# Optimization experiments

Measured on AMD Instinct MI355X. Metric: run time of the kernel, lower is better.

The kernel has to match this reference:

```python
import jax, jax.numpy as jnp
import numpy as np
import math

B, C_IN, C_OUT, W, H = 16, 64, 64, 256, 128
KW = 7  # conv kernel (1, 7), valid padding -> H' = H - 6


def _conv(x, w, b):
    # NCHW input, OIHW weight, valid padding, stride 1 (matches nn.Conv2d)
    y = jax.lax.conv_general_dilated(x, w, (1, 1), 'VALID',
                                     dimension_numbers=('NCHW', 'OIHW', 'NCHW'))
    return y + b[None, :, None, None]


def setup_inputs() -> dict:
    key = jax.random.key(0)
    ks = jax.random.split(key, 7)
    scale = 1.0 / math.sqrt(C_IN * KW)
    x = jax.random.normal(ks[0], (B, C_IN, W, H), jnp.float32)
    wK = jax.random.normal(ks[1], (C_OUT, C_IN, 1, KW), jnp.float32) * scale
    bK = jax.random.normal(ks[2], (C_OUT,), jnp.float32) * scale
    wQ = jax.random.normal(ks[3], (C_OUT, C_IN, 1, KW), jnp.float32) * scale
    bQ = jax.random.normal(ks[4], (C_OUT,), jnp.float32) * scale
    wV = jax.random.normal(ks[5], (C_OUT, C_IN, 1, KW), jnp.float32) * scale
    bV = jax.random.normal(ks[6], (C_OUT,), jnp.float32) * scale
    return {'x': x, 'wK': wK, 'bK': bK, 'wQ': wQ, 'bQ': bQ, 'wV': wV, 'bV': bV}


def reference(x, wK, bK, wQ, bQ, wV, bV):
    b, c, w, h = x.shape
    # raw row-major flatten of NCHW conv output into (B, W, C*H') -- faithful
    # to torch's .reshape(nbatches, w, -1) on a contiguous tensor
    k = _conv(x, wK, bK).reshape(b, w, -1)   # [B, W, C_OUT*(H-6)]
    q = _conv(x, wQ, bQ).reshape(b, w, -1)   # [B, W, C_OUT*(H-6)]
    v = x.reshape(b, w, -1)                  # [B, W, C_IN*H]
    d_k = q.shape[-1]
    scores = jnp.einsum('bqd,bkd->bqk', q, k) / math.sqrt(d_k)  # [B, W, W]
    i = jnp.arange(w)[:, None]
    j = jnp.arange(w)[None, :]
    blocked = ((i < 128) & (j < 128)) | ((i >= 128) & (j >= 128))
    scores = jnp.where(blocked, -jnp.inf, scores)
    p = jax.nn.softmax(scores, axis=-1)
    x1 = jnp.einsum('bqk,bkd->bqd', p, v).reshape(b, c, w, h)
    y = _conv(x1 + x, wV, bV)                # [B, C_OUT, W, H-6]
    return jnp.where(y >= 0, y, 0.2 * y)     # LeakyReLU(0.2)
```

## Files before the change

### kernel.cpp

```cpp
#include <hip/hip_runtime.h>
#include <hip/hip_bf16.h>

using uint32 = unsigned int;
using u16 = unsigned short;
using short8 = __attribute__((ext_vector_type(8))) short;
using f32x4  = __attribute__((ext_vector_type(4))) float;

__device__ __forceinline__ float bf2f(u16 u) {
  union { uint32 i; float f; } c; c.i = ((uint32)u) << 16; return c.f;
}
__device__ __forceinline__ u16 f2bf(float f) {
  union { float f; uint32 i; } c; c.f = f;
  uint32 u = c.i;
  u += 0x7fffu + ((u >> 16) & 1u);
  return (u16)(u >> 16);
}
__device__ __forceinline__ uint32 pack2(float a, float b) {
  return (uint32)f2bf(a) | ((uint32)f2bf(b) << 16);
}

__device__ __forceinline__ void gload_lds16(const void* g, void* l) {
  __builtin_amdgcn_global_load_lds(
      (const __attribute__((address_space(1))) unsigned int*)g,
      (__attribute__((address_space(3))) unsigned int*)l, 16, 0, 0);
}


__global__ __launch_bounds__(256) void prep_weights(
    const float* __restrict__ wK, const float* __restrict__ wQ,
    const float* __restrict__ wV,
    u16* __restrict__ pK, u16* __restrict__ pQ, u16* __restrict__ pV)
{
  int idx = blockIdx.x * 256 + threadIdx.x;
  if (idx >= 86016) return;
  int set = idx / 28672;
  int r = idx - set * 28672;
  int kw = r >> 12;
  int rem = r & 4095;
  int co = rem >> 6, ci = rem & 63;
  const float* src = set == 0 ? wK : (set == 1 ? wQ : wV);
  u16* dst = set == 0 ? pK : (set == 1 ? pQ : pV);
  dst[r] = f2bf(src[co * 448 + ci * 7 + kw]);
}

__global__ __launch_bounds__(256) void prep_x(
    const float* __restrict__ x, u16* __restrict__ xbuf)
{
  __shared__ u16 xt[128 * 64];
  const int bid = blockIdx.x;
  const int b = bid >> 8, w = bid & 255;
  const int t = threadIdx.x;
  const float* xb = x + (size_t)b * 2097152 + (size_t)w * 128;
  #pragma unroll
  for (int it = 0; it < 8; ++it) {
    int idx = t + it * 256;
    int h = idx & 127, gq = idx >> 7;
    int ci0 = gq * 4;
    float v0 = xb[(size_t)(ci0 + 0) * 32768 + h];
    float v1 = xb[(size_t)(ci0 + 1) * 32768 + h];
    float v2 = xb[(size_t)(ci0 + 2) * 32768 + h];
    float v3 = xb[(size_t)(ci0 + 3) * 32768 + h];
    uint2 pk; pk.x = pack2(v0, v1); pk.y = pack2(v2, v3);
    int col = ci0 ^ ((h & 7) << 3);
    *reinterpret_cast<uint2*>(&xt[h * 64 + col]) = pk;
  }
  __syncthreads();
  const uint4* s = reinterpret_cast<const uint4*>(xt);
  uint4* d = reinterpret_cast<uint4*>(xbuf + (size_t)bid * 8192);
  #pragma unroll
  for (int it = 0; it < 4; ++it) d[t + it * 256] = s[t + it * 256];
}

__global__ __launch_bounds__(256) void prep_z(
    const u16* __restrict__ zraw, u16* __restrict__ ztbuf)
{
  __shared__ u16 xt[128 * 64];
  const int bid = blockIdx.x;
  const int b = bid >> 8, w = bid & 255;
  const int t = threadIdx.x;
  const u16* zb = zraw + (size_t)b * 2097152 + (size_t)w * 128;
  #pragma unroll
  for (int it = 0; it < 8; ++it) {
    int idx = t + it * 256;
    int h = idx & 127, gq = idx >> 7;
    int ci0 = gq * 4;
    u16 v0 = zb[(size_t)(ci0 + 0) * 32768 + h];
    u16 v1 = zb[(size_t)(ci0 + 1) * 32768 + h];
    u16 v2 = zb[(size_t)(ci0 + 2) * 32768 + h];
    u16 v3 = zb[(size_t)(ci0 + 3) * 32768 + h];
    uint2 pk;
    pk.x = (uint32)v0 | ((uint32)v1 << 16);
    pk.y = (uint32)v2 | ((uint32)v3 << 16);
    int col = ci0 ^ ((h & 7) << 3);
    *reinterpret_cast<uint2*>(&xt[h * 64 + col]) = pk;
  }
  __syncthreads();
  const uint4* s = reinterpret_cast<const uint4*>(xt);
  uint4* d = reinterpret_cast<uint4*>(ztbuf + (size_t)bid * 8192);
  #pragma unroll
  for (int it = 0; it < 4; ++it) d[t + it * 256] = s[t + it * 256];
}

__global__ __launch_bounds__(256, 4) void conv_kq_mfma(
    const u16* __restrict__ xbuf,
    const u16* __restrict__ wpK, const u16* __restrict__ wpQ,
    const float* __restrict__ bK, const float* __restrict__ bQ,
    u16* __restrict__ qbuf, u16* __restrict__ kbuf)
{
  __shared__ u16 xt[136 * 64];
  const int bid = blockIdx.x;
  const int b = bid >> 8, w = bid & 255;
  const int t = threadIdx.x;
  const int lane = t & 63, wv = t >> 6;
  const int ln = lane & 15, g = lane >> 4;

  {
    const u16* src = xbuf + (size_t)bid * 8192;
    #pragma unroll
    for (int c = 0; c < 4; ++c) {
      int chunk = wv * 4 + c;
      gload_lds16(src + chunk * 512 + lane * 8, &xt[chunk * 512]);
    }
    if (t < 128) {
      *reinterpret_cast<uint2*>(&xt[128 * 64 + t * 4]) = make_uint2(0u, 0u);
    }
  }
  asm volatile("s_waitcnt vmcnt(0)" ::: "memory");
  __syncthreads();

  f32x4 accK[8], accQ[8];
  #pragma unroll
  for (int j = 0; j < 8; ++j) { accK[j] = (f32x4)0.f; accQ[j] = (f32x4)0.f; }

  for (int kw = 0; kw < 7; ++kw) {
    #pragma unroll
    for (int ks = 0; ks < 2; ++ks) {
      const int kb = ks * 32 + g * 8;
      const size_t woff = (size_t)(kw * 64 + wv * 16 + ln) * 64 + kb;
      short8 aK = *reinterpret_cast<const short8*>(wpK + woff);
      short8 aQ = *reinterpret_cast<const short8*>(wpQ + woff);
      #pragma unroll
      for (int j = 0; j < 8; ++j) {
        int row = j * 16 + ln + kw;
        int col = kb ^ ((row & 7) << 3);
        short8 bf = *reinterpret_cast<const short8*>(&xt[row * 64 + col]);
        accK[j] = __builtin_amdgcn_mfma_f32_16x16x32_bf16(aK, bf, accK[j], 0, 0, 0);
        accQ[j] = __builtin_amdgcn_mfma_f32_16x16x32_bf16(aQ, bf, accQ[j], 0, 0, 0);
      }
    }
  }

  #pragma unroll
  for (int r = 0; r < 4; ++r) {
    int co = wv * 16 + g * 4 + r;
    float bk = bK[co], bq = bQ[co];
    size_t base = ((size_t)(b * 64 + co) * 256 + w) * 122;
    #pragma unroll
    for (int j = 0; j < 8; ++j) {
      int n = j * 16 + ln;
      if (n < 122) {
        kbuf[base + n] = f2bf(accK[j][r] + bk);
        qbuf[base + n] = f2bf(accQ[j][r] + bq);
      }
    }
  }
}

__global__ __launch_bounds__(256) void scores_mfma(
    const u16* __restrict__ qbuf, const u16* __restrict__ kbuf,
    u16* __restrict__ pbuf)
{
  __shared__ float lmax[4][16];
  __shared__ float lsum[4][16];
  const int bid = blockIdx.x;
  const int b = bid & 15, rt = bid >> 4;
  const int t = threadIdx.x;
  const int lane = t & 63, wq = t >> 6;
  const int g = lane >> 4, ln = lane & 15;
  const int i0 = rt * 16;
  const int jbase = (rt < 8) ? 128 : 0;

  const u16* qp  = qbuf + (size_t)(b * 256 + i0 + ln) * 7808 + g * 8;
  const u16* kp0 = kbuf + (size_t)(b * 256 + jbase + wq * 32 + ln) * 7808 + g * 8;
  const u16* kp1 = kp0 + (size_t)16 * 7808;

  f32x4 acc0 = (f32x4)0.f, acc1 = (f32x4)0.f;
  #pragma unroll 4
  for (int c = 0; c < 244; ++c) {
    short8 af = *reinterpret_cast<const short8*>(qp + c * 32);
    short8 b0 = *reinterpret_cast<const short8*>(kp0 + c * 32);
    short8 b1 = *reinterpret_cast<const short8*>(kp1 + c * 32);
    acc0 = __builtin_amdgcn_mfma_f32_16x16x32_bf16(af, b0, acc0, 0, 0, 0);
    acc1 = __builtin_amdgcn_mfma_f32_16x16x32_bf16(af, b1, acc1, 0, 0, 0);
  }

  const float scale = 0.011316967f;
  float s0[4], s1[4];
  #pragma unroll
  for (int r = 0; r < 4; ++r) { s0[r] = acc0[r] * scale; s1[r] = acc1[r] * scale; }

  float pm[4], ps[4];
  #pragma unroll
  for (int r = 0; r < 4; ++r) {
    float m = fmaxf(s0[r], s1[r]);
    #pragma unroll
    for (int off = 8; off >= 1; off >>= 1) m = fmaxf(m, __shfl_xor(m, off));
    float e = __expf(s0[r] - m) + __expf(s1[r] - m);
    #pragma unroll
    for (int off = 8; off >= 1; off >>= 1) e += __shfl_xor(e, off);
    pm[r] = m; ps[r] = e;
  }
  if (ln == 0) {
    #pragma unroll
    for (int r = 0; r < 4; ++r) {
      lmax[wq][g * 4 + r] = pm[r];
      lsum[wq][g * 4 + r] = ps[r];
    }
  }
  __syncthreads();

  #pragma unroll
  for (int r = 0; r < 4; ++r) {
    int row = g * 4 + r;
    float m0 = lmax[0][row], m1 = lmax[1][row], m2 = lmax[2][row], m3 = lmax[3][row];
    float mm = fmaxf(fmaxf(m0, m1), fmaxf(m2, m3));
    float ss = lsum[0][row] * __expf(m0 - mm) + lsum[1][row] * __expf(m1 - mm)
             + lsum[2][row] * __expf(m2 - mm) + lsum[3][row] * __expf(m3 - mm);
    float inv = 1.0f / ss;
    float p0 = __expf(s0[r] - mm) * inv;
    float p1 = __expf(s1[r] - mm) * inv;
    u16* prow = pbuf + (size_t)(b * 256 + i0 + row) * 128 + wq * 32 + ln;
    prow[0]  = f2bf(p0);
    prow[16] = f2bf(p1);
  }
}

__global__ __launch_bounds__(256) void pv_mfma(
    const u16* __restrict__ pbuf, const float* __restrict__ x,
    u16* __restrict__ zraw)
{
  __shared__ u16 pl[128 * 136];
  __shared__ u16 vt[256 * 40];
  const int bid = blockIdx.x;
  const int b  = bid >> 6;
  const int hb = (bid >> 5) & 1;
  const int ec = bid & 31;
  const int t = threadIdx.x;
  const int lane = t & 63, wv = t >> 6;
  const int ln = lane & 15, g = lane >> 4;

  const int i0 = hb ? 0 : 128;
  const int jbase = hb ? 128 : 0;
  const int e0 = ec * 256;
  const float* xb = x + (size_t)b * 2097152;

  {
    const u16* pb = pbuf + (size_t)(b * 256 + i0) * 128;
    #pragma unroll
    for (int it = 0; it < 8; ++it) {
      int idx = t + it * 256;
      int row = idx >> 4, c = idx & 15;
      uint4 v = *reinterpret_cast<const uint4*>(pb + row * 128 + c * 8);
      *reinterpret_cast<uint4*>(&pl[row * 136 + c * 8]) = v;
    }
  }

  f32x4 acc[2][16];
  #pragma unroll
  for (int mt = 0; mt < 2; ++mt)
    #pragma unroll
    for (int nt = 0; nt < 16; ++nt) acc[mt][nt] = (f32x4)0.f;

  uint32* vtw = reinterpret_cast<uint32*>(vt);
  for (int ks = 0; ks < 4; ++ks) {
    __syncthreads();
    #pragma unroll
    for (int it = 0; it < 16; ++it) {
      int idx = t + it * 256;
      int e = idx & 255, jp = idx >> 8;
      const float* vr = xb + (size_t)(jbase + ks * 32 + jp * 2) * 8192 + e0 + e;
      float f0 = vr[0];
      float f1 = vr[8192];
      vtw[e * 20 + jp] = pack2(f0, f1);
    }
    __syncthreads();
    short8 af[2];
    #pragma unroll
    for (int mt = 0; mt < 2; ++mt) {
      int row = wv * 32 + mt * 16 + ln;
      af[mt] = *reinterpret_cast<const short8*>(&pl[row * 136 + ks * 32 + g * 8]);
    }
    #pragma unroll
    for (int nt = 0; nt < 16; ++nt) {
      int e = nt * 16 + ln;
      short8 bf = *reinterpret_cast<const short8*>(&vt[e * 40 + g * 8]);
      acc[0][nt] = __builtin_amdgcn_mfma_f32_16x16x32_bf16(af[0], bf, acc[0][nt], 0, 0, 0);
      acc[1][nt] = __builtin_amdgcn_mfma_f32_16x16x32_bf16(af[1], bf, acc[1][nt], 0, 0, 0);
    }
  }

  #pragma unroll
  for (int mt = 0; mt < 2; ++mt) {
    #pragma unroll
    for (int r = 0; r < 4; ++r) {
      int i = i0 + wv * 32 + mt * 16 + g * 4 + r;
      const float* xr = xb + (size_t)i * 8192 + e0 + ln;
      u16* zr = zraw + (size_t)(b * 256 + i) * 8192 + e0 + ln;
      #pragma unroll
      for (int nt = 0; nt < 16; ++nt) {
        float z = xr[nt * 16] + acc[mt][nt][r];
        zr[nt * 16] = f2bf(z);
      }
    }
  }
}

__global__ __launch_bounds__(256, 4) void conv_out_mfma(
    const u16* __restrict__ ztbuf, const u16* __restrict__ wpV,
    const float* __restrict__ bV, float* __restrict__ out)
{
  __shared__ u16 xt[136 * 64];
  const int bid = blockIdx.x;
  const int b = bid >> 8, w = bid & 255;
  const int t = threadIdx.x;
  const int lane = t & 63, wv = t >> 6;
  const int ln = lane & 15, g = lane >> 4;

  {
    const u16* src = ztbuf + (size_t)bid * 8192;
    #pragma unroll
    for (int c = 0; c < 4; ++c) {
      int chunk = wv * 4 + c;
      gload_lds16(src + chunk * 512 + lane * 8, &xt[chunk * 512]);
    }
    if (t < 128) {
      *reinterpret_cast<uint2*>(&xt[128 * 64 + t * 4]) = make_uint2(0u, 0u);
    }
  }
  asm volatile("s_waitcnt vmcnt(0)" ::: "memory");
  __syncthreads();

  f32x4 acc[8];
  #pragma unroll
  for (int j = 0; j < 8; ++j) acc[j] = (f32x4)0.f;

  for (int kw = 0; kw < 7; ++kw) {
    #pragma unroll
    for (int ks = 0; ks < 2; ++ks) {
      const int kb = ks * 32 + g * 8;
      const size_t woff = (size_t)(kw * 64 + wv * 16 + ln) * 64 + kb;
      short8 aV = *reinterpret_cast<const short8*>(wpV + woff);
      #pragma unroll
      for (int j = 0; j < 8; ++j) {
        int row = j * 16 + ln + kw;
        int col = kb ^ ((row & 7) << 3);
        short8 bf = *reinterpret_cast<const short8*>(&xt[row * 64 + col]);
        acc[j] = __builtin_amdgcn_mfma_f32_16x16x32_bf16(aV, bf, acc[j], 0, 0, 0);
      }
    }
  }

  #pragma unroll
  for (int r = 0; r < 4; ++r) {
    int co = wv * 16 + g * 4 + r;
    float bv = bV[co];
    size_t base = ((size_t)(b * 64 + co) * 256 + w) * 122;
    #pragma unroll
    for (int j = 0; j < 8; ++j) {
      int n = j * 16 + ln;
      if (n < 122) {
        float y = acc[j][r] + bv;
        out[base + n] = (y >= 0.f) ? y : 0.2f * y;
      }
    }
  }
}

extern "C" void kernel_launch(void* const* d_in, const int* in_sizes, int n_in,
                              void* d_out, int out_size, void* d_ws, size_t ws_size,
                              hipStream_t stream) {
  const float* x  = (const float*)d_in[0];
  const float* wK = (const float*)d_in[1];
  const float* bK = (const float*)d_in[2];
  const float* wQ = (const float*)d_in[3];
  const float* bQ = (const float*)d_in[4];
  const float* wV = (const float*)d_in[5];
  const float* bV = (const float*)d_in[6];
  float* out = (float*)d_out;

  char* ws = (char*)d_ws;
  u16* qbuf  = (u16*)ws;
  u16* pbuf  = (u16*)(ws + 63963136);
  u16* wpK   = (u16*)(ws + 65011712);
  u16* wpQ   = (u16*)(ws + 65069056);
  u16* kbuf  = (u16*)(ws + 65126400);
  u16* xbuf  = (u16*)(ws + 129089536);
  u16* zraw  = xbuf;
  u16* wpV   = (u16*)(ws + 196198400);
  u16* ztbuf = (u16*)ws;

  prep_weights<<<dim3(336), dim3(256), 0, stream>>>(wK, wQ, wV, wpK, wpQ, wpV);
  prep_x<<<dim3(16 * 256), dim3(256), 0, stream>>>(x, xbuf);
  conv_kq_mfma<<<dim3(16 * 256), dim3(256), 0, stream>>>(xbuf, wpK, wpQ, bK, bQ, qbuf, kbuf);
  scores_mfma<<<dim3(256), dim3(256), 0, stream>>>(qbuf, kbuf, pbuf);
  pv_mfma<<<dim3(1024), dim3(256), 0, stream>>>(pbuf, x, zraw);
  prep_z<<<dim3(16 * 256), dim3(256), 0, stream>>>(zraw, ztbuf);
  conv_out_mfma<<<dim3(16 * 256), dim3(256), 0, stream>>>(ztbuf, wpV, bV, out);
}
```

Measured before the change: 395.1 us.

## Fuse z transpose into PV epilogue and stage conv outputs through LDS

Drops the separate prep_z kernel. The PV kernel now writes its result, already transposed and swizzled, straight into the layout the output convolution consumes, staging each tile through shared memory. The K/Q conv and output conv epilogues also stage results in LDS so that global stores become contiguous wide writes instead of scattered 2-byte and 4-byte stores. This removes a full read and write pass over the z tensor and improves store coalescing, at the cost of extra barriers and LDS traffic in the epilogues. The workspace layout is also reshuffled.

```diff
diff --git a/kernel.cpp b/kernel.cpp
--- a/kernel.cpp
+++ b/kernel.cpp
@@ -67,36 +67,6 @@
   __syncthreads();
   const uint4* s = reinterpret_cast<const uint4*>(xt);
   uint4* d = reinterpret_cast<uint4*>(xbuf + (size_t)bid * 8192);
-  #pragma unroll
-  for (int it = 0; it < 4; ++it) d[t + it * 256] = s[t + it * 256];
-}
-
-__global__ __launch_bounds__(256) void prep_z(
-    const u16* __restrict__ zraw, u16* __restrict__ ztbuf)
-{
-  __shared__ u16 xt[128 * 64];
-  const int bid = blockIdx.x;
-  const int b = bid >> 8, w = bid & 255;
-  const int t = threadIdx.x;
-  const u16* zb = zraw + (size_t)b * 2097152 + (size_t)w * 128;
-  #pragma unroll
-  for (int it = 0; it < 8; ++it) {
-    int idx = t + it * 256;
-    int h = idx & 127, gq = idx >> 7;
-    int ci0 = gq * 4;
-    u16 v0 = zb[(size_t)(ci0 + 0) * 32768 + h];
-    u16 v1 = zb[(size_t)(ci0 + 1) * 32768 + h];
-    u16 v2 = zb[(size_t)(ci0 + 2) * 32768 + h];
-    u16 v3 = zb[(size_t)(ci0 + 3) * 32768 + h];
-    uint2 pk;
-    pk.x = (uint32)v0 | ((uint32)v1 << 16);
-    pk.y = (uint32)v2 | ((uint32)v3 << 16);
-    int col = ci0 ^ ((h & 7) << 3);
-    *reinterpret_cast<uint2*>(&xt[h * 64 + col]) = pk;
-  }
-  __syncthreads();
-  const uint4* s = reinterpret_cast<const uint4*>(xt);
-  uint4* d = reinterpret_cast<uint4*>(ztbuf + (size_t)bid * 8192);
   #pragma unroll
   for (int it = 0; it < 4; ++it) d[t + it * 256] = s[t + it * 256];
 }
@@ -149,20 +119,33 @@
       }
     }
   }
-
-  #pragma unroll
-  for (int r = 0; r < 4; ++r) {
-    int co = wv * 16 + g * 4 + r;
-    float bk = bK[co], bq = bQ[co];
-    size_t base = ((size_t)(b * 64 + co) * 256 + w) * 122;
-    #pragma unroll
-    for (int j = 0; j < 8; ++j) {
-      int n = j * 16 + ln;
-      if (n < 122) {
-        kbuf[base + n] = f2bf(accK[j][r] + bk);
-        qbuf[base + n] = f2bf(accQ[j][r] + bq);
-      }
-    }
+  __syncthreads();
+
+  u16* zs = xt;
+  #pragma unroll
+  for (int p = 0; p < 2; ++p) {
+    #pragma unroll
+    for (int r = 0; r < 4; ++r) {
+      int co = wv * 16 + g * 4 + r;
+      float bias = p ? bQ[co] : bK[co];
+      #pragma unroll
+      for (int j = 0; j < 8; ++j) {
+        int n = j * 16 + ln;
+        if (n < 122)
+          zs[co * 136 + n] = f2bf((p ? accQ[j][r] : accK[j][r]) + bias);
+      }
+    }
+    __syncthreads();
+    const uint32* zw = reinterpret_cast<const uint32*>(zs);
+    uint32* dst = reinterpret_cast<uint32*>(p ? qbuf : kbuf);
+    #pragma unroll
+    for (int pass = 0; pass < 16; ++pass) {
+      int idx = t + pass * 256;
+      int co = idx >> 6, u = idx & 63;
+      if (u < 61)
+        dst[((size_t)(b * 64 + co) * 256 + w) * 61 + u] = zw[co * 68 + u];
+    }
+    __syncthreads();
   }
 }
 
@@ -237,10 +220,11 @@
 
 __global__ __launch_bounds__(256) void pv_mfma(
     const u16* __restrict__ pbuf, const float* __restrict__ x,
-    u16* __restrict__ zraw)
-{
-  __shared__ u16 pl[128 * 136];
-  __shared__ u16 vt[256 * 40];
+    u16* __restrict__ ztbuf)
+{
+  __shared__ u16 smem[27648];
+  u16* pl = smem;
+  u16* vt = smem + 17408;
   const int bid = blockIdx.x;
   const int b  = bid >> 6;
   const int hb = (bid >> 5) & 1;
@@ -299,17 +283,34 @@
     }
   }
 
-  #pragma unroll
-  for (int mt = 0; mt < 2; ++mt) {
-    #pragma unroll
-    for (int r = 0; r < 4; ++r) {
-      int i = i0 + wv * 32 + mt * 16 + g * 4 + r;
-      const float* xr = xb + (size_t)i * 8192 + e0 + ln;
-      u16* zr = zraw + (size_t)(b * 256 + i) * 8192 + e0 + ln;
+  u16* zs = smem;
+  const int cb5 = hb ? 0 : 1;
+  const int cp_base = wv * 8 + g;
+  for (int r = 0; r < 4; ++r) {
+    for (int dwh = 0; dwh < 2; ++dwh) {
+      __syncthreads();
       #pragma unroll
-      for (int nt = 0; nt < 16; ++nt) {
-        float z = xr[nt * 16] + acc[mt][nt][r];
-        zr[nt * 16] = f2bf(z);
+      for (int mt = 0; mt < 2; ++mt) {
+        int i = i0 + wv * 32 + mt * 16 + g * 4 + r;
+        int cp = cp_base + mt * 4;
+        const float* xr = xb + (size_t)i * 8192 + e0 + dwh * 128 + ln;
+        #pragma unroll
+        for (int q = 0; q < 8; ++q) {
+          float z = xr[q * 16] + acc[mt][dwh * 8 + q][r];
+          zs[(q * 16 + ln) * 40 + cp] = f2bf(z);
+        }
+      }
+      __syncthreads();
+      int wimg = r * 64 + ec * 2 + dwh;
+      u16* tb = ztbuf + (size_t)(b * 256 + wimg) * 8192;
+      #pragma unroll
+      for (int pass = 0; pass < 2; ++pass) {
+        int idx = t + pass * 256;
+        int h = idx >> 2, ch = idx & 3;
+        uint4 v = *reinterpret_cast<const uint4*>(&zs[h * 40 + ch * 8]);
+        int blk = 32 * (cb5 ^ ((h >> 2) & 1));
+        int chd = ch ^ (h & 3);
+        *reinterpret_cast<uint4*>(&tb[h * 64 + blk + chd * 8]) = v;
       }
     }
   }
@@ -319,7 +320,8 @@
     const u16* __restrict__ ztbuf, const u16* __restrict__ wpV,
     const float* __restrict__ bV, float* __restrict__ out)
 {
-  __shared__ u16 xt[136 * 64];
+  __shared__ uint32 smem4[8448];
+  u16* xt = reinterpret_cast<u16*>(smem4);
   const int bid = blockIdx.x;
   const int b = bid >> 8, w = bid & 255;
   const int t = threadIdx.x;
@@ -359,19 +361,32 @@
       }
     }
   }
-
+  __syncthreads();
+
+  float* zsf = reinterpret_cast<float*>(smem4);
   #pragma unroll
   for (int r = 0; r < 4; ++r) {
     int co = wv * 16 + g * 4 + r;
     float bv = bV[co];
-    size_t base = ((size_t)(b * 64 + co) * 256 + w) * 122;
     #pragma unroll
     for (int j = 0; j < 8; ++j) {
       int n = j * 16 + ln;
       if (n < 122) {
         float y = acc[j][r] + bv;
-        out[base + n] = (y >= 0.f) ? y : 0.2f * y;
-      }
+        zsf[co * 132 + n] = (y >= 0.f) ? y : 0.2f * y;
+      }
+    }
+  }
+  __syncthreads();
+  const uint2* zw = reinterpret_cast<const uint2*>(zsf);
+  #pragma unroll
+  for (int pass = 0; pass < 16; ++pass) {
+    int idx = t + pass * 256;
+    int co = idx >> 6, u = idx & 63;
+    if (u < 61) {
+      uint2* dst = reinterpret_cast<uint2*>(
+          out + ((size_t)(b * 64 + co) * 256 + w) * 122);
+      dst[u] = zw[co * 66 + u];
     }
   }
 }
@@ -390,20 +405,18 @@
 
   char* ws = (char*)d_ws;
   u16* qbuf  = (u16*)ws;
-  u16* pbuf  = (u16*)(ws + 63963136);
-  u16* wpK   = (u16*)(ws + 65011712);
-  u16* wpQ   = (u16*)(ws + 65069056);
-  u16* kbuf  = (u16*)(ws + 65126400);
-  u16* xbuf  = (u16*)(ws + 129089536);
-  u16* zraw  = xbuf;
-  u16* wpV   = (u16*)(ws + 196198400);
-  u16* ztbuf = (u16*)ws;
+  u16* kbuf  = (u16*)(ws + 63963136);
+  u16* pbuf  = (u16*)(ws + 127926272);
+  u16* wpK   = (u16*)(ws + 128974848);
+  u16* wpQ   = (u16*)(ws + 129032192);
+  u16* wpV   = (u16*)(ws + 129089536);
+  u16* xbuf  = (u16*)(ws + 129146880);
+  u16* ztbuf = xbuf;
 
   prep_weights<<<dim3(336), dim3(256), 0, stream>>>(wK, wQ, wV, wpK, wpQ, wpV);
   prep_x<<<dim3(16 * 256), dim3(256), 0, stream>>>(x, xbuf);
   conv_kq_mfma<<<dim3(16 * 256), dim3(256), 0, stream>>>(xbuf, wpK, wpQ, bK, bQ, qbuf, kbuf);
   scores_mfma<<<dim3(256), dim3(256), 0, stream>>>(qbuf, kbuf, pbuf);
-  pv_mfma<<<dim3(1024), dim3(256), 0, stream>>>(pbuf, x, zraw);
-  prep_z<<<dim3(16 * 256), dim3(256), 0, stream>>>(zraw, ztbuf);
+  pv_mfma<<<dim3(1024), dim3(256), 0, stream>>>(pbuf, x, ztbuf);
   conv_out_mfma<<<dim3(16 * 256), dim3(256), 0, stream>>>(ztbuf, wpV, bV, out);
 }
```

After: 346.2 us. 1.14x faster.
